# Kernel optimization log

Hardware: AMD Instinct MI355X
Metric: run time of the kernel (lower is better)

## Reference

```python
import jax, jax.numpy as jnp
import numpy as np

N = 100000
E = 400000
NFEAT, NHID, NOUT, NHEAD = 128, 64, 128, 4
HIDDEN = NHID * NHEAD  # 256
SLOPE = 0.2


def gat_conv(x, src, dst, W, a_src, a_dst, b, concat):
    """PyG-style GATConv (eval mode, self-loops already appended to src/dst).
    x: [N, Fin]; W: [Fin, H*C]; a_src/a_dst: [H, C]; b: [H*C] or [C]."""
    H, C = a_src.shape
    h = (x @ W).reshape(N, H, C)                      # [N,H,C]
    al_s = (h * a_src).sum(-1)                        # [N,H] per-node src score
    al_d = (h * a_dst).sum(-1)                        # [N,H] per-node dst score
    e = jax.nn.leaky_relu(al_s[src] + al_d[dst], SLOPE)  # [Et,H]
    # segment softmax over incoming edges of each dst node
    m = jax.ops.segment_max(e, dst, num_segments=N)
    m = jnp.where(jnp.isfinite(m), m, 0.0)
    ex = jnp.exp(e - m[dst])
    denom = jax.ops.segment_sum(ex, dst, num_segments=N)
    alpha = ex / (denom[dst] + 1e-16)                 # [Et,H]
    msg = alpha[:, :, None] * h[src]                  # [Et,H,C]
    out = jax.ops.segment_sum(msg, dst, num_segments=N)  # [N,H,C]
    out = out.reshape(N, H * C) if concat else out.mean(axis=1)
    return out + b


def setup_inputs() -> dict:
    key = jax.random.key(0)
    ks = jax.random.split(key, 16)
    x = jax.random.normal(ks[0], (N, NFEAT), dtype=jnp.float32)
    edge_index = jax.random.randint(ks[1], (2, E), 0, N, dtype=jnp.int64)
    s = 0.1
    inp = {
        'x': x, 'edge_index': edge_index,
        # layer 0: nfeat -> nhid x nhead (concat)
        'W0': jax.random.normal(ks[2], (NFEAT, HIDDEN), jnp.float32) * s,
        'as0': jax.random.normal(ks[3], (NHEAD, NHID), jnp.float32) * s,
        'ad0': jax.random.normal(ks[4], (NHEAD, NHID), jnp.float32) * s,
        'b0': jnp.zeros((HIDDEN,), jnp.float32),
        # layer 1: hidden -> nhid x nhead (concat)
        'W1': jax.random.normal(ks[5], (HIDDEN, HIDDEN), jnp.float32) * s,
        'as1': jax.random.normal(ks[6], (NHEAD, NHID), jnp.float32) * s,
        'ad1': jax.random.normal(ks[7], (NHEAD, NHID), jnp.float32) * s,
        'b1': jnp.zeros((HIDDEN,), jnp.float32),
        # output layer: hidden -> nout, heads=1, concat=False
        'W2': jax.random.normal(ks[8], (HIDDEN, NOUT), jnp.float32) * s,
        'as2': jax.random.normal(ks[9], (1, NOUT), jnp.float32) * s,
        'ad2': jax.random.normal(ks[10], (1, NOUT), jnp.float32) * s,
        'b2': jnp.zeros((NOUT,), jnp.float32),
    }
    return inp


def reference(x, edge_index, W0, as0, ad0, b0, W1, as1, ad1, b1, W2, as2, ad2, b2):
    # PyG GATConv adds self-loops by default; edge set is shared across layers.
    loop = jnp.arange(N, dtype=edge_index.dtype)
    src = jnp.concatenate([edge_index[0], loop])
    dst = jnp.concatenate([edge_index[1], loop])
    # dropout inactive in eval mode
    h = jax.nn.elu(gat_conv(x, src, dst, W0, as0, ad0, b0, concat=True))
    h = jax.nn.elu(gat_conv(h, src, dst, W1, as1, ad1, b1, concat=True))
    out = gat_conv(h, src, dst, W2, as2, ad2, b2, concat=False)
    return out
```

## Files before the change

### kernel.cpp

```cpp
#include <hip/hip_runtime.h>
#include <cmath>

#define NN 100000
#define EE 400000
#define SLOPE 0.2f
#define MAXDEG 32

typedef __attribute__((ext_vector_type(8))) short short8;
typedef __attribute__((ext_vector_type(4))) float floatx4;

__device__ __forceinline__ float b2f(ushort u) {
    union { unsigned int i; float f; } v; v.i = ((unsigned int)u) << 16; return v.f;
}
__device__ __forceinline__ ushort f2b(float f) {
    union { float f; unsigned int i; } v; v.f = f;
    unsigned int r = v.i + 0x7FFFu + ((v.i >> 16) & 1u);
    return (ushort)(r >> 16);
}

__device__ __forceinline__ void gload16(const ushort* g, ushort* l) {
    __builtin_amdgcn_global_load_lds((const __attribute__((address_space(1))) void*)g,
                                     (__attribute__((address_space(3))) void*)l, 16, 0, 0);
}

__global__ __launch_bounds__(256) void prep(int* __restrict__ cnt,
                                            float* __restrict__ als2, float* __restrict__ ald2,
                                            const float* __restrict__ W0, const float* __restrict__ W1,
                                            const float* __restrict__ W2,
                                            ushort* __restrict__ Wt0, ushort* __restrict__ Wt1,
                                            ushort* __restrict__ Wt2) {
    int idx = blockIdx.x * 256 + threadIdx.x;
    if (idx < 25000) {
        ((int4*)cnt)[idx] = make_int4(0, 0, 0, 0);
    } else if (idx < 50000) {
        ((float4*)als2)[idx - 25000] = make_float4(0.f, 0.f, 0.f, 0.f);
    } else if (idx < 75000) {
        ((float4*)ald2)[idx - 50000] = make_float4(0.f, 0.f, 0.f, 0.f);
    } else {
        int j = idx - 75000;
        if (j < 32768) {
            int n = j >> 7, k = j & 127;
            Wt0[j] = f2b(W0[(size_t)k * 256 + n]);
        } else if (j < 98304) {
            int t = j - 32768;
            int n = t >> 8, k = t & 255;
            Wt1[t] = f2b(W1[(size_t)k * 256 + n]);
        } else if (j < 131072) {
            int t = j - 98304;
            int n = t >> 8, k = t & 255;
            Wt2[t] = f2b(W2[(size_t)k * 128 + n]);
        }
    }
}

__global__ __launch_bounds__(256) void bucket_scatter(const int* __restrict__ ei,
                                                      int* __restrict__ cnt,
                                                      int* __restrict__ bucket) {
    int e = blockIdx.x * 256 + threadIdx.x;
    if (e < EE) {
        int d = ei[EE + e];
        int p = atomicAdd(&cnt[d], 1);
        if (p < MAXDEG) bucket[(d << 5) + p] = ei[e];
    }
}

template <bool CVT>
__global__ __launch_bounds__(256) void gemm_bf16(const void* __restrict__ Avoid,
                                                 const ushort* __restrict__ Bt,
                                                 ushort* __restrict__ C,
                                                 int M, int K, int N, int paired,
                                                 const float* __restrict__ asf,
                                                 const float* __restrict__ adf,
                                                 float* __restrict__ als,
                                                 float* __restrict__ ald,
                                                 int H, int lgC) {
    __shared__ __attribute__((aligned(16))) ushort As[128 * 64];
    __shared__ __attribute__((aligned(16))) ushort Bs[128 * 64];
    int tid = threadIdx.x;
    int GMc = (M + 127) >> 7;
    int bmi, bni;
    if (paired) {
        int g = blockIdx.x >> 4, ii = blockIdx.x & 15;
        bmi = g * 8 + (ii & 7);
        bni = ii >> 3;
        if (bmi >= GMc) return;
    } else {
        bmi = blockIdx.x; bni = 0;
    }
    int bm = bmi * 128, bn = bni * 128;
    int wave = tid >> 6, lane = tid & 63;
    int wm = (wave >> 1) * 64, wn = (wave & 1) * 64;

    floatx4 acc[4][4];
#pragma unroll
    for (int i = 0; i < 4; i++)
#pragma unroll
        for (int j = 0; j < 4; j++) acc[i][j] = (floatx4)0.f;

    int rsub = lane >> 3;
    int klog8 = ((lane & 7) ^ rsub) * 8;
    ushort* ldsA = &As[wave * 512];
    ushort* ldsB = &Bs[wave * 512];
    const ushort* bS = Bt + (size_t)(bn + wave * 8 + rsub) * K + klog8;
    const ushort* aS = nullptr;
    if (!CVT) aS = (const ushort*)Avoid + (size_t)(bm + wave * 8 + rsub) * K + klog8;

    int frow = lane & 15;
    int q = lane >> 4;
    int f7 = frow & 7;

    for (int k0 = 0; k0 < K; k0 += 64) {
        if constexpr (CVT) {
            const float* Af = (const float*)Avoid;
#pragma unroll
            for (int i = 0; i < 4; i++) {
                int arow = bm + wave * 8 + i * 32 + rsub;
                float4 f0 = make_float4(0.f, 0.f, 0.f, 0.f), f1 = f0;
                if (arow < M) {
                    const float4* ap = (const float4*)(Af + (size_t)arow * K + k0 + klog8);
                    f0 = ap[0]; f1 = ap[1];
                }
                uint4 pk;
                pk.x = (uint)f2b(f0.x) | ((uint)f2b(f0.y) << 16);
                pk.y = (uint)f2b(f0.z) | ((uint)f2b(f0.w) << 16);
                pk.z = (uint)f2b(f1.x) | ((uint)f2b(f1.y) << 16);
                pk.w = (uint)f2b(f1.z) | ((uint)f2b(f1.w) << 16);
                *(uint4*)&ldsA[i * 2048 + lane * 8] = pk;
                gload16(bS + (size_t)i * 32 * K + k0, ldsB + i * 2048);
            }
        } else {
#pragma unroll
            for (int i = 0; i < 4; i++) {
                gload16(aS + (size_t)i * 32 * K + k0, ldsA + i * 2048);
                gload16(bS + (size_t)i * 32 * K + k0, ldsB + i * 2048);
            }
        }
        __syncthreads();

#pragma unroll
        for (int kk = 0; kk < 2; kk++) {
            short8 afr[4], bfr[4];
            int phys = ((kk * 4 + q) ^ f7) * 8;
#pragma unroll
            for (int i = 0; i < 4; i++)
                afr[i] = *(const short8*)&As[(wm + i * 16 + frow) * 64 + phys];
#pragma unroll
            for (int j = 0; j < 4; j++)
                bfr[j] = *(const short8*)&Bs[(wn + j * 16 + frow) * 64 + phys];
#pragma unroll
            for (int i = 0; i < 4; i++)
#pragma unroll
                for (int j = 0; j < 4; j++)
                    acc[i][j] = __builtin_amdgcn_mfma_f32_16x16x32_bf16(afr[i], bfr[j], acc[i][j], 0, 0, 0);
        }
        __syncthreads();
    }

    int ccol = bn + wn + (lane & 15);
    int crow = bm + wm + (lane >> 4) * 4;
#pragma unroll
    for (int i = 0; i < 4; i++) {
#pragma unroll
        for (int reg = 0; reg < 4; reg++) {
            int row = crow + i * 16 + reg;
            if (row < M) {
#pragma unroll
                for (int j = 0; j < 4; j++)
                    C[(size_t)row * N + ccol + j * 16] = f2b(acc[i][j][reg]);
            }
        }
    }

    {
        int cb = bn + wn + (lane & 15);
        float asv[4], adv[4];
#pragma unroll
        for (int j = 0; j < 4; j++) {
            asv[j] = asf[cb + j * 16];
            adv[j] = adf[cb + j * 16];
        }
        int hidx = (bn + wn) >> lgC;
#pragma unroll
        for (int i = 0; i < 4; i++) {
#pragma unroll
            for (int reg = 0; reg < 4; reg++) {
                float ss = acc[i][0][reg] * asv[0] + acc[i][1][reg] * asv[1]
                         + acc[i][2][reg] * asv[2] + acc[i][3][reg] * asv[3];
                float dd = acc[i][0][reg] * adv[0] + acc[i][1][reg] * adv[1]
                         + acc[i][2][reg] * adv[2] + acc[i][3][reg] * adv[3];
#pragma unroll
                for (int off = 1; off < 16; off <<= 1) {
                    ss += __shfl_xor(ss, off, 64);
                    dd += __shfl_xor(dd, off, 64);
                }
                int row = crow + i * 16 + reg;
                if ((lane & 15) == 0 && row < M) {
                    if (lgC == 6) {
                        als[row * H + hidx] = ss;
                        ald[row * H + hidx] = dd;
                    } else {
                        atomicAdd(&als[row], ss);
                        atomicAdd(&ald[row], dd);
                    }
                }
            }
        }
    }
}

template <int H, int HC, bool ELU_ACT, bool OUT_BF16>
__global__ __launch_bounds__(256) void aggregate(const ushort* __restrict__ hlin,
                                                 const float* __restrict__ als,
                                                 const float* __restrict__ ald,
                                                 const int* __restrict__ cnt,
                                                 const int* __restrict__ bucket,
                                                 const float* __restrict__ bias,
                                                 void* __restrict__ outv) {
    constexpr int CP = HC / 64;
    constexpr int GS = 64 / H;
    int wv = threadIdx.x >> 6, lane = threadIdx.x & 63;
    int dst = blockIdx.x * 4 + wv;
    if (dst >= NN) return;
    int deg = min(cnt[dst], MAXDEG);
    int dtot = deg + 1;
    int rs = dst << 5;
    int eg = lane & (GS - 1);
    int head = lane / GS;
    float ad = ald[dst * H + head];

    float acc[CP];
#pragma unroll
    for (int j = 0; j < CP; j++) acc[j] = 0.f;

    uint laneoff = (uint)(lane * CP);

    if (dtot <= GS) {
        int src = 0;
        float s = -1e30f;
        if (eg < dtot) {
            src = (eg < deg) ? bucket[rs + eg] : dst;
            float sc = als[src * H + head] + ad;
            s = sc > 0.f ? sc : SLOPE * sc;
        }
        float m = s;
#pragma unroll
        for (int off = 1; off < GS; off <<= 1) m = fmaxf(m, __shfl_xor(m, off, 64));
        float e = (eg < dtot) ? __expf(s - m) : 0.f;
        float sum = e;
#pragma unroll
        for (int off = 1; off < GS; off <<= 1) sum += __shfl_xor(sum, off, 64);
        float w = e * (1.0f / (sum + 1e-16f));

        int hbase = head * GS;
        int d = 0;
        for (; d + 4 <= dtot; d += 4) {
            int s0 = __shfl(src, d, 64),     s1 = __shfl(src, d + 1, 64);
            int s2 = __shfl(src, d + 2, 64), s3 = __shfl(src, d + 3, 64);
            float w0 = __shfl(w, hbase + d, 64),     w1 = __shfl(w, hbase + d + 1, 64);
            float w2 = __shfl(w, hbase + d + 2, 64), w3 = __shfl(w, hbase + d + 3, 64);
            const uint* p0 = (const uint*)(hlin + (uint)s0 * HC + laneoff);
            const uint* p1 = (const uint*)(hlin + (uint)s1 * HC + laneoff);
            const uint* p2 = (const uint*)(hlin + (uint)s2 * HC + laneoff);
            const uint* p3 = (const uint*)(hlin + (uint)s3 * HC + laneoff);
            uint u0[CP / 2], u1[CP / 2], u2[CP / 2], u3[CP / 2];
#pragma unroll
            for (int qq = 0; qq < CP / 2; qq++) { u0[qq] = p0[qq]; u1[qq] = p1[qq]; u2[qq] = p2[qq]; u3[qq] = p3[qq]; }
#pragma unroll
            for (int qq = 0; qq < CP / 2; qq++) {
                acc[2*qq]   += w0 * b2f((ushort)(u0[qq] & 0xffff)) + w1 * b2f((ushort)(u1[qq] & 0xffff))
                             + w2 * b2f((ushort)(u2[qq] & 0xffff)) + w3 * b2f((ushort)(u3[qq] & 0xffff));
                acc[2*qq+1] += w0 * b2f((ushort)(u0[qq] >> 16)) + w1 * b2f((ushort)(u1[qq] >> 16))
                             + w2 * b2f((ushort)(u2[qq] >> 16)) + w3 * b2f((ushort)(u3[qq] >> 16));
            }
        }
        for (; d < dtot; d++) {
            int sd = __shfl(src, d, 64);
            float wd = __shfl(w, hbase + d, 64);
            const uint* p = (const uint*)(hlin + (uint)sd * HC + laneoff);
#pragma unroll
            for (int qq = 0; qq < CP / 2; qq++) {
                uint u = p[qq];
                acc[2*qq]   += wd * b2f((ushort)(u & 0xffff));
                acc[2*qq+1] += wd * b2f((ushort)(u >> 16));
            }
        }
    } else {
        float m = -1e30f;
        for (int e2 = eg; e2 < dtot; e2 += GS) {
            int s0 = (e2 < deg) ? bucket[rs + e2] : dst;
            float sc = als[s0 * H + head] + ad;
            sc = sc > 0.f ? sc : SLOPE * sc;
            m = fmaxf(m, sc);
        }
#pragma unroll
        for (int off = 1; off < GS; off <<= 1) m = fmaxf(m, __shfl_xor(m, off, 64));
        float sum = 0.f;
        for (int e2 = eg; e2 < dtot; e2 += GS) {
            int s0 = (e2 < deg) ? bucket[rs + e2] : dst;
            float sc = als[s0 * H + head] + ad;
            sc = sc > 0.f ? sc : SLOPE * sc;
            sum += __expf(sc - m);
        }
#pragma unroll
        for (int off = 1; off < GS; off <<= 1) sum += __shfl_xor(sum, off, 64);
        float inv = 1.0f / (sum + 1e-16f);
        for (int d = 0; d < dtot; d++) {
            int sd = (d < deg) ? bucket[rs + d] : dst;
            float sc = als[sd * H + head] + ad;
            sc = sc > 0.f ? sc : SLOPE * sc;
            float wd = __expf(sc - m) * inv;
            const uint* p = (const uint*)(hlin + (uint)sd * HC + laneoff);
#pragma unroll
            for (int qq = 0; qq < CP / 2; qq++) {
                uint u = p[qq];
                acc[2*qq]   += wd * b2f((ushort)(u & 0xffff));
                acc[2*qq+1] += wd * b2f((ushort)(u >> 16));
            }
        }
    }

#pragma unroll
    for (int j = 0; j < CP; j++) {
        float v = acc[j] + bias[lane * CP + j];
        if (ELU_ACT) v = v > 0.f ? v : (__expf(v) - 1.0f);
        acc[j] = v;
    }
    if (OUT_BF16) {
        ushort* outp = (ushort*)outv + (size_t)dst * HC + laneoff;
        uint pk[CP / 2];
#pragma unroll
        for (int qq = 0; qq < CP / 2; qq++)
            pk[qq] = (uint)f2b(acc[2*qq]) | ((uint)f2b(acc[2*qq+1]) << 16);
#pragma unroll
        for (int qq = 0; qq < CP / 2; qq++) ((uint*)outp)[qq] = pk[qq];
    } else {
        float* outp = (float*)outv + (size_t)dst * HC + laneoff;
#pragma unroll
        for (int j = 0; j < CP; j++) outp[j] = acc[j];
    }
}

extern "C" void kernel_launch(void* const* d_in, const int* in_sizes, int n_in,
                              void* d_out, int out_size, void* d_ws, size_t ws_size,
                              hipStream_t stream) {
    const float* x   = (const float*)d_in[0];
    const int*   ei  = (const int*)d_in[1];
    const float* W0  = (const float*)d_in[2];
    const float* as0 = (const float*)d_in[3];
    const float* ad0 = (const float*)d_in[4];
    const float* b0  = (const float*)d_in[5];
    const float* W1  = (const float*)d_in[6];
    const float* as1 = (const float*)d_in[7];
    const float* ad1 = (const float*)d_in[8];
    const float* b1  = (const float*)d_in[9];
    const float* W2  = (const float*)d_in[10];
    const float* as2 = (const float*)d_in[11];
    const float* ad2 = (const float*)d_in[12];
    const float* b2  = (const float*)d_in[13];
    float* out = (float*)d_out;

    char* ws = (char*)d_ws;
    size_t off = 0;
    auto alloc = [&](size_t bytes) {
        void* p = ws + off;
        off += (bytes + 255) & ~(size_t)255;
        return p;
    };
    ushort* h    = (ushort*)alloc((size_t)NN * 256 * 2);
    ushort* actB = (ushort*)alloc((size_t)(NN + 128) * 256 * 2);
    ushort* actC = (ushort*)alloc((size_t)(NN + 128) * 256 * 2);
    ushort* Wt0  = (ushort*)alloc((size_t)256 * 128 * 2);
    ushort* Wt1  = (ushort*)alloc((size_t)256 * 256 * 2);
    ushort* Wt2  = (ushort*)alloc((size_t)128 * 256 * 2);
    float* als   = (float*)alloc((size_t)NN * 4 * 4);
    float* ald   = (float*)alloc((size_t)NN * 4 * 4);
    float* als2  = (float*)alloc((size_t)NN * 4);
    float* ald2  = (float*)alloc((size_t)NN * 4);
    int* cnt     = (int*)alloc((size_t)NN * 4);
    int* bucket  = (int*)alloc((size_t)NN * MAXDEG * 4);

    prep<<<(75000 + 131072 + 255) / 256, 256, 0, stream>>>(cnt, als2, ald2, W0, W1, W2, Wt0, Wt1, Wt2);

    bucket_scatter<<<(EE + 255) / 256, 256, 0, stream>>>(ei, cnt, bucket);

    const int GMc = (NN + 127) / 128;
    const int GPAIR = 16 * ((GMc + 7) / 8);
    const int NB4 = (NN + 3) / 4;

    gemm_bf16<true><<<GPAIR, 256, 0, stream>>>(x, Wt0, h, NN, 128, 256, 1, as0, ad0, als, ald, 4, 6);
    aggregate<4, 256, true, true><<<NB4, 256, 0, stream>>>(h, als, ald, cnt, bucket, b0, actB);

    gemm_bf16<false><<<GPAIR, 256, 0, stream>>>(actB, Wt1, h, NN, 256, 256, 1, as1, ad1, als, ald, 4, 6);
    aggregate<4, 256, true, true><<<NB4, 256, 0, stream>>>(h, als, ald, cnt, bucket, b1, actC);

    gemm_bf16<false><<<GMc, 256, 0, stream>>>(actC, Wt2, h, NN, 256, 128, 0, as2, ad2, als2, ald2, 1, 7);
    aggregate<1, 128, false, false><<<NB4, 256, 0, stream>>>(h, als2, ald2, cnt, bucket, b2, out);
}
```

Baseline: 412.4 us.

## Double-buffer GEMM LDS tiles to overlap next-tile loads with MFMA compute

Doubles the A and B shared-memory tiles and prefetches the next K-tile, either by direct global-to-LDS loads or by register loads followed by bf16 conversion, while MFMAs run on the current tile. This drops one barrier per iteration and hides global-load latency behind compute. In exchange it doubles LDS use to 64KB per block, which may reduce occupancy, and raises register pressure in the CVT path. With K of only 128 or 256 there are just 2 to 4 tiles, so there is little to overlap, and the GEMM is only part of the total time.

Result: no change. 420.6 us (+2.0%).

```diff
diff --git a/kernel.cpp b/kernel.cpp
--- a/kernel.cpp
+++ b/kernel.cpp
@@ -74,8 +74,8 @@
                                                  float* __restrict__ als,
                                                  float* __restrict__ ald,
                                                  int H, int lgC) {
-    __shared__ __attribute__((aligned(16))) ushort As[128 * 64];
-    __shared__ __attribute__((aligned(16))) ushort Bs[128 * 64];
+    __shared__ __attribute__((aligned(16))) ushort As[2 * 128 * 64];
+    __shared__ __attribute__((aligned(16))) ushort Bs[2 * 128 * 64];
     int tid = threadIdx.x;
     int GMc = (M + 127) >> 7;
     int bmi, bni;
@@ -104,56 +104,106 @@
     const ushort* bS = Bt + (size_t)(bn + wave * 8 + rsub) * K + klog8;
     const ushort* aS = nullptr;
     if (!CVT) aS = (const ushort*)Avoid + (size_t)(bm + wave * 8 + rsub) * K + klog8;
+    const float* Af = (const float*)Avoid;
 
     int frow = lane & 15;
     int q = lane >> 4;
     int f7 = frow & 7;
 
-    for (int k0 = 0; k0 < K; k0 += 64) {
+    int nt = K >> 6;
+    int cur = 0;
+
+    if constexpr (CVT) {
+#pragma unroll
+        for (int i = 0; i < 4; i++) {
+            int arow = bm + wave * 8 + i * 32 + rsub;
+            float4 f0 = make_float4(0.f, 0.f, 0.f, 0.f), f1 = f0;
+            if (arow < M) {
+                const float4* ap = (const float4*)(Af + (size_t)arow * K + klog8);
+                f0 = ap[0]; f1 = ap[1];
+            }
+            uint4 pk;
+            pk.x = (uint)f2b(f0.x) | ((uint)f2b(f0.y) << 16);
+            pk.y = (uint)f2b(f0.z) | ((uint)f2b(f0.w) << 16);
+            pk.z = (uint)f2b(f1.x) | ((uint)f2b(f1.y) << 16);
+            pk.w = (uint)f2b(f1.z) | ((uint)f2b(f1.w) << 16);
+            *(uint4*)&ldsA[i * 2048 + lane * 8] = pk;
+            gload16(bS + (size_t)i * 32 * K, ldsB + i * 2048);
+        }
+    } else {
+#pragma unroll
+        for (int i = 0; i < 4; i++) {
+            gload16(aS + (size_t)i * 32 * K, ldsA + i * 2048);
+            gload16(bS + (size_t)i * 32 * K, ldsB + i * 2048);
+        }
+    }
+    __syncthreads();
+
+    for (int t = 0; t < nt; t++) {
+        bool pre = (t + 1 < nt);
+        int k0n = (t + 1) << 6;
+        int nofs = (cur ^ 1) * 8192;
+
+        float4 g0[4], g1[4];
         if constexpr (CVT) {
-            const float* Af = (const float*)Avoid;
-#pragma unroll
-            for (int i = 0; i < 4; i++) {
-                int arow = bm + wave * 8 + i * 32 + rsub;
-                float4 f0 = make_float4(0.f, 0.f, 0.f, 0.f), f1 = f0;
-                if (arow < M) {
-                    const float4* ap = (const float4*)(Af + (size_t)arow * K + k0 + klog8);
-                    f0 = ap[0]; f1 = ap[1];
+            if (pre) {
+#pragma unroll
+                for (int i = 0; i < 4; i++) {
+                    int arow = bm + wave * 8 + i * 32 + rsub;
+                    g0[i] = make_float4(0.f, 0.f, 0.f, 0.f); g1[i] = g0[i];
+                    if (arow < M) {
+                        const float4* ap = (const float4*)(Af + (size_t)arow * K + k0n + klog8);
+                        g0[i] = ap[0]; g1[i] = ap[1];
+                    }
+                    gload16(bS + (size_t)i * 32 * K + k0n, ldsB + nofs + i * 2048);
                 }
-                uint4 pk;
-                pk.x = (uint)f2b(f0.x) | ((uint)f2b(f0.y) << 16);
-                pk.y = (uint)f2b(f0.z) | ((uint)f2b(f0.w) << 16);
-                pk.z = (uint)f2b(f1.x) | ((uint)f2b(f1.y) << 16);
-                pk.w = (uint)f2b(f1.z) | ((uint)f2b(f1.w) << 16);
-                *(uint4*)&ldsA[i * 2048 + lane * 8] = pk;
-                gload16(bS + (size_t)i * 32 * K + k0, ldsB + i * 2048);
             }
         } else {
-#pragma unroll
-            for (int i = 0; i < 4; i++) {
-                gload16(aS + (size_t)i * 32 * K + k0, ldsA + i * 2048);
-                gload16(bS + (size_t)i * 32 * K + k0, ldsB + i * 2048);
-            }
-        }
+            if (pre) {
+#pragma unroll
+                for (int i = 0; i < 4; i++) {
+                    gload16(aS + (size_t)i * 32 * K + k0n, ldsA + nofs + i * 2048);
+                    gload16(bS + (size_t)i * 32 * K + k0n, ldsB + nofs + i * 2048);
+                }
+            }
+        }
+
+        {
+            int bofs = cur * 8192;
+#pragma unroll
+            for (int kk = 0; kk < 2; kk++) {
+                short8 afr[4], bfr[4];
+                int phys = ((kk * 4 + q) ^ f7) * 8;
+#pragma unroll
+                for (int i = 0; i < 4; i++)
+                    afr[i] = *(const short8*)&As[bofs + (wm + i * 16 + frow) * 64 + phys];
+#pragma unroll
+                for (int j = 0; j < 4; j++)
+                    bfr[j] = *(const short8*)&Bs[bofs + (wn + j * 16 + frow) * 64 + phys];
+#pragma unroll
+                for (int i = 0; i < 4; i++)
+#pragma unroll
+                    for (int j = 0; j < 4; j++)
+                        acc[i][j] = __builtin_amdgcn_mfma_f32_16x16x32_bf16(afr[i], bfr[j], acc[i][j], 0, 0, 0);
+            }
+        }
+
+        if constexpr (CVT) {
+            if (pre) {
+#pragma unroll
+                for (int i = 0; i < 4; i++) {
+                    uint4 pk;
+                    pk.x = (uint)f2b(g0[i].x) | ((uint)f2b(g0[i].y) << 16);
+                    pk.y = (uint)f2b(g0[i].z) | ((uint)f2b(g0[i].w) << 16);
+                    pk.z = (uint)f2b(g1[i].x) | ((uint)f2b(g1[i].y) << 16);
+                    pk.w = (uint)f2b(g1[i].z) | ((uint)f2b(g1[i].w) << 16);
+                    *(uint4*)&ldsA[nofs + i * 2048 + lane * 8] = pk;
+                }
+            }
+        }
+
         __syncthreads();
-
-#pragma unroll
-        for (int kk = 0; kk < 2; kk++) {
-            short8 afr[4], bfr[4];
-            int phys = ((kk * 4 + q) ^ f7) * 8;
-#pragma unroll
-            for (int i = 0; i < 4; i++)
-                afr[i] = *(const short8*)&As[(wm + i * 16 + frow) * 64 + phys];
-#pragma unroll
-            for (int j = 0; j < 4; j++)
-                bfr[j] = *(const short8*)&Bs[(wn + j * 16 + frow) * 64 + phys];
-#pragma unroll
-            for (int i = 0; i < 4; i++)
-#pragma unroll
-                for (int j = 0; j < 4; j++)
-                    acc[i][j] = __builtin_amdgcn_mfma_f32_16x16x32_bf16(afr[i], bfr[j], acc[i][j], 0, 0, 0);
-        }
-        __syncthreads();
+        cur ^= 1;
     }
 
     int ccol = bn + wn + (lane & 15);
```

## Widen GEMM tiles to full output width with 512-thread blocks

Applied to the files above, without the earlier changes.

Templates the projection GEMM on tile sizes and runs 8-wave blocks. Layers 0 and 1 use 128x256 tiles, so each block covers the full output width and the A tile is loaded and converted only once instead of once per column half. The last layer uses 256x128 tiles. This replaces the paired two-block column split and makes K compile-time, in exchange for larger LDS use per block and fewer blocks in the grid.

New measurement: 412.8 us. Within noise of the previous version (+0.1%).

```diff
diff --git a/kernel.cpp b/kernel.cpp
--- a/kernel.cpp
+++ b/kernel.cpp
@@ -64,32 +64,26 @@
     }
 }
 
-template <bool CVT>
-__global__ __launch_bounds__(256) void gemm_bf16(const void* __restrict__ Avoid,
+template <bool CVT, int BM, int BN, int KK>
+__global__ __launch_bounds__(512) void gemm_bf16(const void* __restrict__ Avoid,
                                                  const ushort* __restrict__ Bt,
                                                  ushort* __restrict__ C,
-                                                 int M, int K, int N, int paired,
+                                                 int M,
                                                  const float* __restrict__ asf,
                                                  const float* __restrict__ adf,
                                                  float* __restrict__ als,
                                                  float* __restrict__ ald,
                                                  int H, int lgC) {
-    __shared__ __attribute__((aligned(16))) ushort As[128 * 64];
-    __shared__ __attribute__((aligned(16))) ushort Bs[128 * 64];
+    constexpr int NSA = BM / 64;
+    constexpr int NSB = BN / 64;
+    constexpr int NCW = BN / 64;
+    __shared__ __attribute__((aligned(16))) ushort As[BM * 64];
+    __shared__ __attribute__((aligned(16))) ushort Bs[BN * 64];
     int tid = threadIdx.x;
-    int GMc = (M + 127) >> 7;
-    int bmi, bni;
-    if (paired) {
-        int g = blockIdx.x >> 4, ii = blockIdx.x & 15;
-        bmi = g * 8 + (ii & 7);
-        bni = ii >> 3;
-        if (bmi >= GMc) return;
-    } else {
-        bmi = blockIdx.x; bni = 0;
-    }
-    int bm = bmi * 128, bn = bni * 128;
     int wave = tid >> 6, lane = tid & 63;
-    int wm = (wave >> 1) * 64, wn = (wave & 1) * 64;
+    int wrow = wave / NCW, wcol = wave % NCW;
+    int wm = wrow * 64, wn = wcol * 64;
+    int bm = blockIdx.x * BM;
 
     floatx4 acc[4][4];
 #pragma unroll
@@ -99,25 +93,21 @@
 
     int rsub = lane >> 3;
     int klog8 = ((lane & 7) ^ rsub) * 8;
-    ushort* ldsA = &As[wave * 512];
-    ushort* ldsB = &Bs[wave * 512];
-    const ushort* bS = Bt + (size_t)(bn + wave * 8 + rsub) * K + klog8;
-    const ushort* aS = nullptr;
-    if (!CVT) aS = (const ushort*)Avoid + (size_t)(bm + wave * 8 + rsub) * K + klog8;
-
     int frow = lane & 15;
     int q = lane >> 4;
     int f7 = frow & 7;
 
-    for (int k0 = 0; k0 < K; k0 += 64) {
+    const float*  Af = (const float*)Avoid;
+    const ushort* Ab = (const ushort*)Avoid;
+
+    for (int k0 = 0; k0 < KK; k0 += 64) {
         if constexpr (CVT) {
-            const float* Af = (const float*)Avoid;
-#pragma unroll
-            for (int i = 0; i < 4; i++) {
-                int arow = bm + wave * 8 + i * 32 + rsub;
+#pragma unroll
+            for (int i = 0; i < NSA; i++) {
+                int arow = bm + (wave + 8 * i) * 8 + rsub;
                 float4 f0 = make_float4(0.f, 0.f, 0.f, 0.f), f1 = f0;
                 if (arow < M) {
-                    const float4* ap = (const float4*)(Af + (size_t)arow * K + k0 + klog8);
+                    const float4* ap = (const float4*)(Af + (size_t)arow * KK + k0 + klog8);
                     f0 = ap[0]; f1 = ap[1];
                 }
                 uint4 pk;
@@ -125,16 +115,19 @@
                 pk.y = (uint)f2b(f0.z) | ((uint)f2b(f0.w) << 16);
                 pk.z = (uint)f2b(f1.x) | ((uint)f2b(f1.y) << 16);
                 pk.w = (uint)f2b(f1.z) | ((uint)f2b(f1.w) << 16);
-                *(uint4*)&ldsA[i * 2048 + lane * 8] = pk;
-                gload16(bS + (size_t)i * 32 * K + k0, ldsB + i * 2048);
+                *(uint4*)&As[(wave + 8 * i) * 512 + lane * 8] = pk;
             }
         } else {
 #pragma unroll
-            for (int i = 0; i < 4; i++) {
-                gload16(aS + (size_t)i * 32 * K + k0, ldsA + i * 2048);
-                gload16(bS + (size_t)i * 32 * K + k0, ldsB + i * 2048);
-            }
-        }
+            for (int i = 0; i < NSA; i++)
+                gload16(Ab + (size_t)(bm + (wave + 8 * i) * 8 + rsub) * KK + k0 + klog8,
+                        &As[(wave + 8 * i) * 512]);
+        }
+#pragma unroll
+        for (int i = 0; i < NSB; i++)
+            gload16(Bt + (size_t)((wave + 8 * i) * 8 + rsub) * KK + k0 + klog8,
+                    &Bs[(wave + 8 * i) * 512]);
+
         __syncthreads();
 
 #pragma unroll
@@ -156,7 +149,7 @@
         __syncthreads();
     }
 
-    int ccol = bn + wn + (lane & 15);
+    int ccol = wn + (lane & 15);
     int crow = bm + wm + (lane >> 4) * 4;
 #pragma unroll
     for (int i = 0; i < 4; i++) {
@@ -166,20 +159,19 @@
             if (row < M) {
 #pragma unroll
                 for (int j = 0; j < 4; j++)
-                    C[(size_t)row * N + ccol + j * 16] = f2b(acc[i][j][reg]);
+                    C[(size_t)row * BN + ccol + j * 16] = f2b(acc[i][j][reg]);
             }
         }
     }
 
     {
-        int cb = bn + wn + (lane & 15);
         float asv[4], adv[4];
 #pragma unroll
         for (int j = 0; j < 4; j++) {
-            asv[j] = asf[cb + j * 16];
-            adv[j] = adf[cb + j * 16];
-        }
-        int hidx = (bn + wn) >> lgC;
+            asv[j] = asf[wn + (lane & 15) + j * 16];
+            adv[j] = adf[wn + (lane & 15) + j * 16];
+        }
+        int hidx = wn >> 6;
 #pragma unroll
         for (int i = 0; i < 4; i++) {
 #pragma unroll
@@ -367,8 +359,8 @@
         return p;
     };
     ushort* h    = (ushort*)alloc((size_t)NN * 256 * 2);
-    ushort* actB = (ushort*)alloc((size_t)(NN + 128) * 256 * 2);
-    ushort* actC = (ushort*)alloc((size_t)(NN + 128) * 256 * 2);
+    ushort* actB = (ushort*)alloc((size_t)(NN + 256) * 256 * 2);
+    ushort* actC = (ushort*)alloc((size_t)(NN + 256) * 256 * 2);
     ushort* Wt0  = (ushort*)alloc((size_t)256 * 128 * 2);
     ushort* Wt1  = (ushort*)alloc((size_t)256 * 256 * 2);
     ushort* Wt2  = (ushort*)alloc((size_t)128 * 256 * 2);
@@ -383,16 +375,16 @@
 
     bucket_scatter<<<(EE + 255) / 256, 256, 0, stream>>>(ei, cnt, bucket);
 
-    const int GMc = (NN + 127) / 128;
-    const int GPAIR = 16 * ((GMc + 7) / 8);
+    const int GM128 = (NN + 127) / 128;
+    const int GM256 = (NN + 255) / 256;
     const int NB4 = (NN + 3) / 4;
 
-    gemm_bf16<true><<<GPAIR, 256, 0, stream>>>(x, Wt0, h, NN, 128, 256, 1, as0, ad0, als, ald, 4, 6);
+    gemm_bf16<true, 128, 256, 128><<<GM128, 512, 0, stream>>>(x, Wt0, h, NN, as0, ad0, als, ald, 4, 6);
     aggregate<4, 256, true, true><<<NB4, 256, 0, stream>>>(h, als, ald, cnt, bucket, b0, actB);
 
-    gemm_bf16<false><<<GPAIR, 256, 0, stream>>>(actB, Wt1, h, NN, 256, 256, 1, as1, ad1, als, ald, 4, 6);
+    gemm_bf16<false, 128, 256, 256><<<GM128, 512, 0, stream>>>(actB, Wt1, h, NN, as1, ad1, als, ald, 4, 6);
     aggregate<4, 256, true, true><<<NB4, 256, 0, stream>>>(h, als, ald, cnt, bucket, b1, actC);
 
-    gemm_bf16<false><<<GMc, 256, 0, stream>>>(actC, Wt2, h, NN, 256, 128, 0, as2, ad2, als2, ald2, 1, 7);
+    gemm_bf16<false, 256, 128, 256><<<GM256, 512, 0, stream>>>(actC, Wt2, h, NN, as2, ad2, als2, ald2, 1, 7);
     aggregate<1, 128, false, false><<<NB4, 256, 0, stream>>>(h, als2, ald2, cnt, bucket, b2, out);
 }
```
